# Optimization experiments

Measured on AMD Instinct MI355X. Metric: run time of the kernel, lower is better.

Reference implementation:

```python
import jax, jax.numpy as jnp
import numpy as np
from itertools import combinations

EPS = 1e-5

# flattened channel-pair index list: 36 pairs of the 9 GLCM shift channels -> 72 indices
PAIRS = np.asarray(list(combinations(range(9), 2)), dtype=np.int32).reshape(-1)


def glcm_stack(img):
    # img: [B,1,H,W]; replicate torch slice+cat shifts exactly (edge rows/cols duplicated)
    left = lambda a: jnp.concatenate([a[:, :, :, 1:], a[:, :, :, -1:]], axis=3)
    up = lambda a: jnp.concatenate([a[:, :, 1:, :], a[:, :, -1:, :]], axis=2)
    down = lambda a: jnp.concatenate([a[:, :, :1, :], a[:, :, :-1, :]], axis=2)
    right = lambda a: jnp.concatenate([a[:, :, :, :1], a[:, :, :, :-1]], axis=3)
    gl3, gl6, gl7, gl8 = left(img), up(img), down(img), down(img)
    return jnp.concatenate([
        img, left(img), up(img), up(gl3), right(img),
        down(img), left(gl6), left(gl7), right(gl8)], axis=1)  # [B,9,H,W]


def bn(x, gamma, beta, mean, var):
    scale = (gamma / jnp.sqrt(var + EPS))[:, None, None]
    return (x - mean[:, None, None]) * scale + beta[:, None, None]


def setup_inputs() -> dict:
    key = jax.random.key(0)
    ks = jax.random.split(key, 8)
    n = 36
    x = jax.random.normal(ks[0], (32, 64, 224, 224), dtype=jnp.float32)
    gw = jax.random.normal(ks[1], (n, 2), dtype=jnp.float32) * 0.5      # grouped 1x1 conv [out=n, in/group=2]
    w1 = jax.random.normal(ks[2], (n, n), dtype=jnp.float32) * 0.1      # 1x1 conv n->n
    ca_w1 = jax.random.normal(ks[3], (n // 2, n), dtype=jnp.float32) * 0.2
    ca_w2 = jax.random.normal(ks[4], (n, n // 2), dtype=jnp.float32) * 0.2
    bng_g = jnp.ones((n,), jnp.float32); bng_b = jnp.zeros((n,), jnp.float32)
    bng_m = jax.random.normal(ks[5], (n,), dtype=jnp.float32) * 0.1
    bng_v = jnp.abs(jax.random.normal(ks[6], (n,), dtype=jnp.float32)) + 0.5
    bn1_g = jnp.ones((n,), jnp.float32); bn1_b = jnp.zeros((n,), jnp.float32)
    bn1_m = jax.random.normal(ks[7], (n,), dtype=jnp.float32) * 0.1
    bn1_v = jnp.ones((n,), jnp.float32)
    return dict(x=x, gw=gw, w1=w1, ca_w1=ca_w1, ca_w2=ca_w2,
                bng_g=bng_g, bng_b=bng_b, bng_m=bng_m, bng_v=bng_v,
                bn1_g=bn1_g, bn1_b=bn1_b, bn1_m=bn1_m, bn1_v=bn1_v)


def reference(x, gw, w1, ca_w1, ca_w2, bng_g, bng_b, bng_m, bng_v,
              bn1_g, bn1_b, bn1_m, bn1_v):
    avgout = jnp.mean(x, axis=1, keepdims=True)            # [B,1,H,W]
    g = glcm_stack(avgout)                                 # [B,9,H,W]
    B, _, H, W = g.shape
    feas = jnp.take(g, jnp.asarray(PAIRS), axis=1)         # [B,72,H,W]
    feas = feas.reshape(B, 36, 2, H, W)
    y = jnp.einsum('bgchw,gc->bghw', feas, gw)             # grouped 1x1 conv
    y = jax.nn.relu(bn(y, bng_g, bng_b, bng_m, bng_v))
    y = jnp.einsum('bchw,oc->bohw', y, w1)                 # 1x1 conv n->n
    y = bn(y, bn1_g, bn1_b, bn1_m, bn1_v)
    pooled = jnp.mean(y, axis=(2, 3))                      # [B,36]
    att = jax.nn.sigmoid(jax.nn.relu(pooled @ ca_w1.T) @ ca_w2.T)  # [B,36]
    y = y * att[:, :, None, None]
    out = jax.nn.sigmoid(jnp.sum(y, axis=1, keepdims=True))  # [B,1,H,W]
    return out
```

## Files before the change

kernel.cpp:

```cpp
#include <hip/hip_runtime.h>
#include <math.h>

#define B_   32
#define C_   64
#define H_   224
#define W_   224
#define HW_  (H_*W_)
#define HW4_ (HW_/4)
#define G_   36
#define CHUNKS_ 28
#define ROWS_ 8
#define SEGW_ 7

typedef float f4v __attribute__((ext_vector_type(4)));

__global__ __launch_bounds__(256) void k_mean(const float* __restrict__ x,
                                              float* __restrict__ a) {
    int b = blockIdx.x / 49;
    int i = (blockIdx.x % 49) * 256 + threadIdx.x;
    const f4v* x4 = reinterpret_cast<const f4v*>(x) + (size_t)b * C_ * HW4_ + i;
    f4v s = {0.f, 0.f, 0.f, 0.f};
    #pragma unroll 8
    for (int c = 0; c < C_; ++c) {
        s += x4[(size_t)c * HW4_];
    }
    s *= (1.0f / 64.0f);
    reinterpret_cast<f4v*>(a)[(size_t)b * HW4_ + i] = s;
}

#define PAIR_LIST(OP) \
  OP(0,0,1) OP(1,0,2) OP(2,0,3) OP(3,0,4) OP(4,0,5) OP(5,0,6) OP(6,0,7) OP(7,0,8) \
  OP(8,1,2) OP(9,1,3) OP(10,1,4) OP(11,1,5) OP(12,1,6) OP(13,1,7) OP(14,1,8) \
  OP(15,2,3) OP(16,2,4) OP(17,2,5) OP(18,2,6) OP(19,2,7) OP(20,2,8) \
  OP(21,3,4) OP(22,3,5) OP(23,3,6) OP(24,3,7) OP(25,3,8) \
  OP(26,4,5) OP(27,4,6) OP(28,4,7) OP(29,4,8) \
  OP(30,5,6) OP(31,5,7) OP(32,5,8) \
  OP(33,6,7) OP(34,6,8) OP(35,7,8)

#define STAGE_BAND() do { \
    const f4v* ab4 = reinterpret_cast<const f4v*>(a + (size_t)b * HW_); \
    _Pragma("unroll") \
    for (int k = 0; k < 3; ++k) { \
        int q = k * 256 + t; \
        if (q < 10 * (W_/4)) { \
            int row = q / (W_/4); \
            int c4  = q - row * (W_/4); \
            int gr = r0 - 1 + row; \
            gr = gr < 0 ? 0 : (gr > H_-1 ? H_-1 : gr); \
            *reinterpret_cast<f4v*>(&sm[row * W_ + c4 * 4]) = ab4[gr * (W_/4) + c4]; \
        } \
    } } while (0)


__global__ __launch_bounds__(256) void k_sums(const float* __restrict__ a,
                                              const float* __restrict__ gw,
                                              const float* __restrict__ bng_g, const float* __restrict__ bng_b,
                                              const float* __restrict__ bng_m, const float* __restrict__ bng_v,
                                              float* __restrict__ partial) {
    int b = blockIdx.x / CHUNKS_;
    int chunk = blockIdx.x % CHUNKS_;
    int t = threadIdx.x;
    __shared__ float sA0[G_], sA1[G_], sB[G_];
    __shared__ float sm[10 * W_];
    __shared__ float red[4 * G_];
    if (t < G_) {
        float sg = bng_g[t] / sqrtf(bng_v[t] + 1e-5f);
        sA0[t] = gw[2*t+0] * sg;
        sA1[t] = gw[2*t+1] * sg;
        sB[t]  = bng_b[t] - bng_m[t] * sg;
    }
    int r0 = chunk * ROWS_;
    STAGE_BAND();
    __syncthreads();

    int seg = t & 31, lr = t >> 5;
    int w0 = seg * SEGW_;
    const float* RU = &sm[lr * W_];
    const float* RC = &sm[(lr+1) * W_];
    const float* RD = &sm[(lr+2) * W_];

    #define LOADC(g,i0,i1) float A0##g = sA0[g], A1##g = sA1[g], Bc##g = sB[g];
    PAIR_LIST(LOADC)
    #undef LOADC
    #define DECLACC(g,i0,i1) float acc##g = 0.f;
    PAIR_LIST(DECLACC)
    #undef DECLACC

    int cI = w0 > 0 ? w0 - 1 : 0;
    float uL = RU[cI], cl_ = RC[cI];
    float uC = RU[w0], cc_ = RC[w0], dC = RD[w0];
    #pragma unroll
    for (int j = 0; j < SEGW_; ++j) {
        int cR = w0 + j + 1; cR = cR < W_ ? cR : W_ - 1;
        float uR = RU[cR], cr_ = RC[cR], dR = RD[cR];
        float n0 = cc_, n1 = cr_, n2 = dC, n3 = dR, n4 = cl_,
              n5 = uC, n6 = dR, n7 = uR, n8 = uL;
        #define SUM_OP(g,i0,i1) acc##g += fmaxf(fmaf(A0##g, n##i0, fmaf(A1##g, n##i1, Bc##g)), 0.f);
        PAIR_LIST(SUM_OP)
        #undef SUM_OP
        uL = uC; cl_ = cc_; uC = uR; cc_ = cr_; dC = dR;
    }

    int lane = t & 63, wave = t >> 6;
    #define RED_OP(g,i0,i1) { float v = acc##g; \
        v += __shfl_down(v, 32); v += __shfl_down(v, 16); v += __shfl_down(v, 8); \
        v += __shfl_down(v, 4);  v += __shfl_down(v, 2);  v += __shfl_down(v, 1); \
        if (lane == 0) red[wave * G_ + g] = v; }
    PAIR_LIST(RED_OP)
    #undef RED_OP
    __syncthreads();
    if (t < G_) {
        partial[(size_t)(b * CHUNKS_ + chunk) * G_ + t] =
            red[t] + red[G_+t] + red[2*G_+t] + red[3*G_+t];
    }
}

__global__ void k_att(const float* __restrict__ partial,
                      const float* __restrict__ bn1_g, const float* __restrict__ bn1_b,
                      const float* __restrict__ bn1_m, const float* __restrict__ bn1_v,
                      const float* __restrict__ w1, const float* __restrict__ ca_w1,
                      const float* __restrict__ ca_w2,
                      float* __restrict__ vout, float* __restrict__ cout) {
    int b = blockIdx.x;
    int t = threadIdx.x;
    __shared__ float ss1[G_], sb1[G_];
    __shared__ float meanr[G_], pooled[G_], hid[G_/2], att[G_];
    if (t < G_) {
        float s1 = bn1_g[t] / sqrtf(bn1_v[t] + 1e-5f);
        ss1[t] = s1;
        sb1[t] = bn1_b[t] - bn1_m[t] * s1;
        float s = 0.f;
        for (int j = 0; j < CHUNKS_; ++j) s += partial[(size_t)(b * CHUNKS_ + j) * G_ + t];
        meanr[t] = s * (1.0f / (float)HW_);
    }
    __syncthreads();
    if (t < G_) {
        float s = 0.f;
        #pragma unroll
        for (int g = 0; g < G_; ++g) s += w1[t*G_ + g] * meanr[g];
        pooled[t] = fmaf(s, ss1[t], sb1[t]);
    }
    __syncthreads();
    if (t < G_/2) {
        float s = 0.f;
        #pragma unroll
        for (int o = 0; o < G_; ++o) s += pooled[o] * ca_w1[t*G_ + o];
        hid[t] = fmaxf(s, 0.f);
    }
    __syncthreads();
    if (t < G_) {
        float s = 0.f;
        #pragma unroll
        for (int k = 0; k < G_/2; ++k) s += hid[k] * ca_w2[t*(G_/2) + k];
        att[t] = 1.0f / (1.0f + expf(-s));
    }
    __syncthreads();
    if (t < G_) {
        float s = 0.f;
        #pragma unroll
        for (int o = 0; o < G_; ++o) s += att[o] * ss1[o] * w1[o*G_ + t];
        vout[b*G_ + t] = s;
    }
    if (t == 63) {
        float s = 0.f;
        #pragma unroll
        for (int o = 0; o < G_; ++o) s += att[o] * sb1[o];
        cout[b] = s;
    }
}

__global__ __launch_bounds__(256) void k_out(const float* __restrict__ a,
                                             const float* __restrict__ gw,
                                             const float* __restrict__ bng_g, const float* __restrict__ bng_b,
                                             const float* __restrict__ bng_m, const float* __restrict__ bng_v,
                                             const float* __restrict__ v,
                                             const float* __restrict__ cvals,
                                             float* __restrict__ out) {
    int b = blockIdx.x / CHUNKS_;
    int chunk = blockIdx.x % CHUNKS_;
    int t = threadIdx.x;
    __shared__ float sA0[G_], sA1[G_], sB[G_], sV[G_];
    __shared__ float sm[10 * W_];
    __shared__ float sC;
    if (t < G_) {
        float sg = bng_g[t] / sqrtf(bng_v[t] + 1e-5f);
        sA0[t] = gw[2*t+0] * sg;
        sA1[t] = gw[2*t+1] * sg;
        sB[t]  = bng_b[t] - bng_m[t] * sg;
        sV[t]  = v[b*G_ + t];
    }
    if (t == 63) sC = cvals[b];
    int r0 = chunk * ROWS_;
    STAGE_BAND();
    __syncthreads();

    int seg = t & 31, lr = t >> 5;
    int w0 = seg * SEGW_;
    const float* RU = &sm[lr * W_];
    const float* RC = &sm[(lr+1) * W_];
    const float* RD = &sm[(lr+2) * W_];
    float* ob = out + (size_t)b * HW_ + (r0 + lr) * W_;

    #define LOADC(g,i0,i1) float A0##g = sA0[g], A1##g = sA1[g], Bc##g = sB[g], V##g = sV[g];
    PAIR_LIST(LOADC)
    #undef LOADC
    float c0 = sC;

    int cI = w0 > 0 ? w0 - 1 : 0;
    float uL = RU[cI], cl_ = RC[cI];
    float uC = RU[w0], cc_ = RC[w0], dC = RD[w0];
    #pragma unroll
    for (int j = 0; j < SEGW_; ++j) {
        int cR = w0 + j + 1; cR = cR < W_ ? cR : W_ - 1;
        float uR = RU[cR], cr_ = RC[cR], dR = RD[cR];
        float n0 = cc_, n1 = cr_, n2 = dC, n3 = dR, n4 = cl_,
              n5 = uC, n6 = dR, n7 = uR, n8 = uL;
        float s = c0;
        #define OUT_OP(g,i0,i1) s = fmaf(fmaxf(fmaf(A0##g, n##i0, fmaf(A1##g, n##i1, Bc##g)), 0.f), V##g, s);
        PAIR_LIST(OUT_OP)
        #undef OUT_OP
        ob[w0 + j] = 1.0f / (1.0f + expf(-s));
        uL = uC; cl_ = cc_; uC = uR; cc_ = cr_; dC = dR;
    }
}

extern "C" void kernel_launch(void* const* d_in, const int* in_sizes, int n_in,
                              void* d_out, int out_size, void* d_ws, size_t ws_size,
                              hipStream_t stream) {
    const float* x     = (const float*)d_in[0];
    const float* gw    = (const float*)d_in[1];
    const float* w1    = (const float*)d_in[2];
    const float* ca_w1 = (const float*)d_in[3];
    const float* ca_w2 = (const float*)d_in[4];
    const float* bng_g = (const float*)d_in[5];
    const float* bng_b = (const float*)d_in[6];
    const float* bng_m = (const float*)d_in[7];
    const float* bng_v = (const float*)d_in[8];
    const float* bn1_g = (const float*)d_in[9];
    const float* bn1_b = (const float*)d_in[10];
    const float* bn1_m = (const float*)d_in[11];
    const float* bn1_v = (const float*)d_in[12];

    float* ws      = (float*)d_ws;
    float* a       = ws;
    float* partial = a + (size_t)B_ * HW_;
    float* v       = partial + (size_t)B_ * CHUNKS_ * G_;
    float* cvals   = v + B_ * G_;

    k_mean<<<B_ * 49, 256, 0, stream>>>(x, a);
    k_sums<<<B_ * CHUNKS_, 256, 0, stream>>>(a, gw,
        bng_g, bng_b, bng_m, bng_v, partial);
    k_att<<<B_, 64, 0, stream>>>(partial,
        bn1_g, bn1_b, bn1_m, bn1_v, w1, ca_w1, ca_w2, v, cvals);
    k_out<<<B_ * CHUNKS_, 256, 0, stream>>>(a, gw,
        bng_g, bng_b, bng_m, bng_v, v, cvals, (float*)d_out);
}
```

Measured before the change: 121.6 us.

## Fuse attention MLP into output kernel and use LDS transpose reduction in k_sums

Removes the separate tiny k_att launch by having every k_out block recompute the per-batch channel-attention vector from the partial sums before its main loop. This drops one kernel launch and its serialization gap, at the cost of redundant small MLP work and extra barriers in each of the 896 output blocks. In k_sums, the 36 per-accumulator wave shuffle reductions are replaced by writing accumulators to a padded LDS buffer and summing columns with 144 threads. That enlarges shared memory to about 37 KB per block, which may reduce occupancy.

```diff
diff --git a/kernel.cpp b/kernel.cpp
--- a/kernel.cpp
+++ b/kernel.cpp
@@ -37,7 +37,7 @@
   OP(30,5,6) OP(31,5,7) OP(32,5,8) \
   OP(33,6,7) OP(34,6,8) OP(35,7,8)
 
-#define STAGE_BAND() do { \
+#define STAGE_BAND(bufp) do { \
     const f4v* ab4 = reinterpret_cast<const f4v*>(a + (size_t)b * HW_); \
     _Pragma("unroll") \
     for (int k = 0; k < 3; ++k) { \
@@ -47,7 +47,7 @@
             int c4  = q - row * (W_/4); \
             int gr = r0 - 1 + row; \
             gr = gr < 0 ? 0 : (gr > H_-1 ? H_-1 : gr); \
-            *reinterpret_cast<f4v*>(&sm[row * W_ + c4 * 4]) = ab4[gr * (W_/4) + c4]; \
+            *reinterpret_cast<f4v*>(&(bufp)[row * W_ + c4 * 4]) = ab4[gr * (W_/4) + c4]; \
         } \
     } } while (0)
 
@@ -61,8 +61,8 @@
     int chunk = blockIdx.x % CHUNKS_;
     int t = threadIdx.x;
     __shared__ float sA0[G_], sA1[G_], sB[G_];
-    __shared__ float sm[10 * W_];
-    __shared__ float red[4 * G_];
+    __shared__ float buf[256 * 37];
+    __shared__ float red2[4 * G_];
     if (t < G_) {
         float sg = bng_g[t] / sqrtf(bng_v[t] + 1e-5f);
         sA0[t] = gw[2*t+0] * sg;
@@ -70,14 +70,14 @@
         sB[t]  = bng_b[t] - bng_m[t] * sg;
     }
     int r0 = chunk * ROWS_;
-    STAGE_BAND();
+    STAGE_BAND(buf);
     __syncthreads();
 
     int seg = t & 31, lr = t >> 5;
     int w0 = seg * SEGW_;
-    const float* RU = &sm[lr * W_];
-    const float* RC = &sm[(lr+1) * W_];
-    const float* RD = &sm[(lr+2) * W_];
+    const float* RU = &buf[lr * W_];
+    const float* RC = &buf[(lr+1) * W_];
+    const float* RD = &buf[(lr+2) * W_];
 
     #define LOADC(g,i0,i1) float A0##g = sA0[g], A1##g = sA1[g], Bc##g = sB[g];
     PAIR_LIST(LOADC)
@@ -101,97 +101,90 @@
         uL = uC; cl_ = cc_; uC = uR; cc_ = cr_; dC = dR;
     }
 
-    int lane = t & 63, wave = t >> 6;
-    #define RED_OP(g,i0,i1) { float v = acc##g; \
-        v += __shfl_down(v, 32); v += __shfl_down(v, 16); v += __shfl_down(v, 8); \
-        v += __shfl_down(v, 4);  v += __shfl_down(v, 2);  v += __shfl_down(v, 1); \
-        if (lane == 0) red[wave * G_ + g] = v; }
-    PAIR_LIST(RED_OP)
-    #undef RED_OP
+    __syncthreads();
+    #define WR_OP(g,i0,i1) buf[t * 37 + g] = acc##g;
+    PAIR_LIST(WR_OP)
+    #undef WR_OP
+    __syncthreads();
+    if (t < 4 * G_) {
+        int g = t >> 2, q = t & 3;
+        float s = 0.f;
+        int base = q * 64;
+        for (int i = 0; i < 64; ++i) s += buf[(base + i) * 37 + g];
+        red2[g * 4 + q] = s;
+    }
     __syncthreads();
     if (t < G_) {
         partial[(size_t)(b * CHUNKS_ + chunk) * G_ + t] =
-            red[t] + red[G_+t] + red[2*G_+t] + red[3*G_+t];
-    }
-}
-
-__global__ void k_att(const float* __restrict__ partial,
-                      const float* __restrict__ bn1_g, const float* __restrict__ bn1_b,
-                      const float* __restrict__ bn1_m, const float* __restrict__ bn1_v,
-                      const float* __restrict__ w1, const float* __restrict__ ca_w1,
-                      const float* __restrict__ ca_w2,
-                      float* __restrict__ vout, float* __restrict__ cout) {
-    int b = blockIdx.x;
-    int t = threadIdx.x;
-    __shared__ float ss1[G_], sb1[G_];
-    __shared__ float meanr[G_], pooled[G_], hid[G_/2], att[G_];
-    if (t < G_) {
-        float s1 = bn1_g[t] / sqrtf(bn1_v[t] + 1e-5f);
-        ss1[t] = s1;
-        sb1[t] = bn1_b[t] - bn1_m[t] * s1;
-        float s = 0.f;
-        for (int j = 0; j < CHUNKS_; ++j) s += partial[(size_t)(b * CHUNKS_ + j) * G_ + t];
-        meanr[t] = s * (1.0f / (float)HW_);
-    }
-    __syncthreads();
-    if (t < G_) {
-        float s = 0.f;
-        #pragma unroll
-        for (int g = 0; g < G_; ++g) s += w1[t*G_ + g] * meanr[g];
-        pooled[t] = fmaf(s, ss1[t], sb1[t]);
-    }
-    __syncthreads();
-    if (t < G_/2) {
-        float s = 0.f;
-        #pragma unroll
-        for (int o = 0; o < G_; ++o) s += pooled[o] * ca_w1[t*G_ + o];
-        hid[t] = fmaxf(s, 0.f);
-    }
-    __syncthreads();
-    if (t < G_) {
-        float s = 0.f;
-        #pragma unroll
-        for (int k = 0; k < G_/2; ++k) s += hid[k] * ca_w2[t*(G_/2) + k];
-        att[t] = 1.0f / (1.0f + expf(-s));
-    }
-    __syncthreads();
-    if (t < G_) {
-        float s = 0.f;
-        #pragma unroll
-        for (int o = 0; o < G_; ++o) s += att[o] * ss1[o] * w1[o*G_ + t];
-        vout[b*G_ + t] = s;
-    }
-    if (t == 63) {
-        float s = 0.f;
-        #pragma unroll
-        for (int o = 0; o < G_; ++o) s += att[o] * sb1[o];
-        cout[b] = s;
+            red2[4*t] + red2[4*t+1] + red2[4*t+2] + red2[4*t+3];
     }
 }
 
 __global__ __launch_bounds__(256) void k_out(const float* __restrict__ a,
+                                             const float* __restrict__ partial,
                                              const float* __restrict__ gw,
                                              const float* __restrict__ bng_g, const float* __restrict__ bng_b,
                                              const float* __restrict__ bng_m, const float* __restrict__ bng_v,
-                                             const float* __restrict__ v,
-                                             const float* __restrict__ cvals,
+                                             const float* __restrict__ bn1_g, const float* __restrict__ bn1_b,
+                                             const float* __restrict__ bn1_m, const float* __restrict__ bn1_v,
+                                             const float* __restrict__ w1, const float* __restrict__ ca_w1,
+                                             const float* __restrict__ ca_w2,
                                              float* __restrict__ out) {
     int b = blockIdx.x / CHUNKS_;
     int chunk = blockIdx.x % CHUNKS_;
     int t = threadIdx.x;
     __shared__ float sA0[G_], sA1[G_], sB[G_], sV[G_];
+    __shared__ float ss1[G_], sb1[G_], meanr[G_], pooled[G_], hid[G_/2], att[G_];
     __shared__ float sm[10 * W_];
-    __shared__ float sC;
+    __shared__ float sCv[1];
     if (t < G_) {
         float sg = bng_g[t] / sqrtf(bng_v[t] + 1e-5f);
         sA0[t] = gw[2*t+0] * sg;
         sA1[t] = gw[2*t+1] * sg;
         sB[t]  = bng_b[t] - bng_m[t] * sg;
-        sV[t]  = v[b*G_ + t];
-    }
-    if (t == 63) sC = cvals[b];
+        float s1 = bn1_g[t] / sqrtf(bn1_v[t] + 1e-5f);
+        ss1[t] = s1;
+        sb1[t] = bn1_b[t] - bn1_m[t] * s1;
+        float s = 0.f;
+        for (int j = 0; j < CHUNKS_; ++j) s += partial[(size_t)(b * CHUNKS_ + j) * G_ + t];
+        meanr[t] = s * (1.0f / (float)HW_);
+    }
     int r0 = chunk * ROWS_;
-    STAGE_BAND();
+    STAGE_BAND(sm);
+    __syncthreads();
+    if (t < G_) {
+        float s = 0.f;
+        #pragma unroll
+        for (int g = 0; g < G_; ++g) s += w1[t*G_ + g] * meanr[g];
+        pooled[t] = fmaf(s, ss1[t], sb1[t]);
+    }
+    __syncthreads();
+    if (t < G_/2) {
+        float s = 0.f;
+        #pragma unroll
+        for (int o = 0; o < G_; ++o) s += pooled[o] * ca_w1[t*G_ + o];
+        hid[t] = fmaxf(s, 0.f);
+    }
+    __syncthreads();
+    if (t < G_) {
+        float s = 0.f;
+        #pragma unroll
+        for (int k = 0; k < G_/2; ++k) s += hid[k] * ca_w2[t*(G_/2) + k];
+        att[t] = 1.0f / (1.0f + expf(-s));
+    }
+    __syncthreads();
+    if (t < G_) {
+        float s = 0.f;
+        #pragma unroll
+        for (int o = 0; o < G_; ++o) s += att[o] * ss1[o] * w1[o*G_ + t];
+        sV[t] = s;
+    }
+    if (t == 63) {
+        float s = 0.f;
+        #pragma unroll
+        for (int o = 0; o < G_; ++o) s += att[o] * sb1[o];
+        sCv[0] = s;
+    }
     __syncthreads();
 
     int seg = t & 31, lr = t >> 5;
@@ -204,7 +197,7 @@
     #define LOADC(g,i0,i1) float A0##g = sA0[g], A1##g = sA1[g], Bc##g = sB[g], V##g = sV[g];
     PAIR_LIST(LOADC)
     #undef LOADC
-    float c0 = sC;
+    float c0 = sCv[0];
 
     int cI = w0 > 0 ? w0 - 1 : 0;
     float uL = RU[cI], cl_ = RC[cI];
@@ -244,14 +237,11 @@
     float* ws      = (float*)d_ws;
     float* a       = ws;
     float* partial = a + (size_t)B_ * HW_;
-    float* v       = partial + (size_t)B_ * CHUNKS_ * G_;
-    float* cvals   = v + B_ * G_;
 
     k_mean<<<B_ * 49, 256, 0, stream>>>(x, a);
     k_sums<<<B_ * CHUNKS_, 256, 0, stream>>>(a, gw,
         bng_g, bng_b, bng_m, bng_v, partial);
-    k_att<<<B_, 64, 0, stream>>>(partial,
-        bn1_g, bn1_b, bn1_m, bn1_v, w1, ca_w1, ca_w2, v, cvals);
-    k_out<<<B_ * CHUNKS_, 256, 0, stream>>>(a, gw,
-        bng_g, bng_b, bng_m, bng_v, v, cvals, (float*)d_out);
-}
+    k_out<<<B_ * CHUNKS_, 256, 0, stream>>>(a, partial, gw,
+        bng_g, bng_b, bng_m, bng_v, bn1_g, bn1_b, bn1_m, bn1_v,
+        w1, ca_w1, ca_w2, (float*)d_out);
+}
```

Result: faster. 113.3 us (-6.8%).
